# Kernel optimization log

Hardware: AMD Instinct MI355X
Metric: run time of the kernel (lower is better)

Reference implementation:

```python
import jax, jax.numpy as jnp
import numpy as np

HIDDEN = 1024

def _init_linear(key, in_f, out_f):
    kw, kb = jax.random.split(key)
    bound = 1.0 / np.sqrt(in_f)
    W = jax.random.uniform(kw, (out_f, in_f), jnp.float32, -bound, bound)
    b = jax.random.uniform(kb, (out_f,), jnp.float32, -bound, bound)
    return W, b

def setup_inputs() -> dict:
    key = jax.random.key(0)
    ks = jax.random.split(key, 6)
    x = jax.random.normal(ks[0], (64, 512, 512), jnp.float32)
    # layer 0: input_size=512, hidden=1024
    W_rz0, b_rz0 = _init_linear(ks[1], 512 + HIDDEN, 2 * HIDDEN)
    W_n0, b_n0 = _init_linear(ks[2], 512 + HIDDEN, HIDDEN)
    # layer 1: input_size=hidden=1024
    W_rz1, b_rz1 = _init_linear(ks[3], HIDDEN + HIDDEN, 2 * HIDDEN)
    W_n1, b_n1 = _init_linear(ks[4], HIDDEN + HIDDEN, HIDDEN)
    # final fc: hidden -> output_size=512
    W_fc, b_fc = _init_linear(ks[5], HIDDEN, 512)
    return {"x": x, "W_rz0": W_rz0, "b_rz0": b_rz0, "W_n0": W_n0, "b_n0": b_n0,
            "W_rz1": W_rz1, "b_rz1": b_rz1, "W_n1": W_n1, "b_n1": b_n1,
            "W_fc": W_fc, "b_fc": b_fc}

def _gru_cell(xt, h, W_rz, b_rz, W_n, b_n):
    ih = jnp.concatenate([xt, h], axis=1)                 # [B, in+H]
    rz = ih @ W_rz.T + b_rz                               # [B, 2H]
    r, z = jnp.split(rz, 2, axis=1)
    r = jax.nn.sigmoid(r)
    z = jax.nn.sigmoid(z)
    ih_n = jnp.concatenate([xt, r * h], axis=1)
    n = jnp.tanh(ih_n @ W_n.T + b_n)
    return (1.0 - z) * n + z * h

def reference(x, W_rz0, b_rz0, W_n0, b_n0, W_rz1, b_rz1, W_n1, b_n1, W_fc, b_fc):
    B = x.shape[0]
    h0 = jnp.zeros((B, HIDDEN), x.dtype)
    h1 = jnp.zeros((B, HIDDEN), x.dtype)

    def step(carry, xt):
        h0, h1 = carry
        h0 = _gru_cell(xt, h0, W_rz0, b_rz0, W_n0, b_n0)
        h1 = _gru_cell(h0, h1, W_rz1, b_rz1, W_n1, b_n1)
        return (h0, h1), None

    xs = jnp.swapaxes(x, 0, 1)                            # [T, B, in]
    (h0, h1), _ = jax.lax.scan(step, (h0, h1), xs)
    # original returns outputs[:, -1, :] == fc(final hidden of last layer)
    return h1 @ W_fc.T + b_fc
```

## Files before the change

### kernel.cpp

```cpp
#include <hip/hip_runtime.h>
#include <math.h>

typedef _Float16 h8 __attribute__((ext_vector_type(8)));
typedef float f4 __attribute__((ext_vector_type(4)));

#define H 1024

#define OFF_WRZ0 0ull
#define OFF_WN0  6291456ull
#define OFF_WRZ1 9437184ull
#define OFF_WN1  17825792ull
#define OFF_H0BF 22020096ull
#define OFF_H1BF 22282240ull
#define OFF_RH0  22544384ull
#define OFF_RH1  22675456ull
#define OFF_H0F  22806528ull
#define OFF_H1F  23068672ull
#define OFF_Z0F  23330816ull
#define OFF_Z1F  23592960ull
#define OFF_CNT  23855104ull
#define OFF_INFO 23856128ull
#define OFF_CCNT 23857152ull
#define OFF_CP   23863296ull
#define CP_XCD_STRIDE 655360ull
#define ZERO_WORDS 460800

__device__ __forceinline__ unsigned long long llc_ld64(const void* p) {
  return __hip_atomic_load((const unsigned long long*)p, __ATOMIC_RELAXED, __HIP_MEMORY_SCOPE_AGENT);
}
__device__ __forceinline__ void llc_st64(void* p, unsigned long long v) {
  __hip_atomic_store((unsigned long long*)p, v, __ATOMIC_RELAXED, __HIP_MEMORY_SCOPE_AGENT);
}
__device__ __forceinline__ void llc_st32(void* p, unsigned v) {
  __hip_atomic_store((unsigned*)p, v, __ATOMIC_RELAXED, __HIP_MEMORY_SCOPE_AGENT);
}
__device__ __forceinline__ unsigned long long pack2f(float a, float b) {
  union { float f[2]; unsigned long long u; } x; x.f[0] = a; x.f[1] = b; return x.u;
}
__device__ __forceinline__ void unpack2f(unsigned long long v, float& a, float& b) {
  union { unsigned long long u; float f[2]; } x; x.u = v; a = x.f[0]; b = x.f[1];
}
__device__ __forceinline__ unsigned packh2(float a, float b) {
  union { _Float16 h[2]; unsigned u; } x; x.h[0] = (_Float16)a; x.h[1] = (_Float16)b; return x.u;
}

__global__ __launch_bounds__(256) void prep_kernel(
    const float* __restrict__ wrz0f, const float* __restrict__ wn0f,
    const float* __restrict__ wrz1f, const float* __restrict__ wn1f,
    _Float16* __restrict__ wrz0, _Float16* __restrict__ wn0,
    _Float16* __restrict__ wrz1, _Float16* __restrict__ wn1,
    unsigned* __restrict__ zbase) {
  size_t i = (size_t)blockIdx.x * blockDim.x + threadIdx.x;
  size_t stride = (size_t)gridDim.x * blockDim.x;
  for (size_t k = i; k < 2048ull * 1536ull; k += stride) wrz0[k] = (_Float16)wrz0f[k];
  for (size_t k = i; k < 1024ull * 1536ull; k += stride) wn0[k]  = (_Float16)wn0f[k];
  for (size_t k = i; k < 2048ull * 2048ull; k += stride) wrz1[k] = (_Float16)wrz1f[k];
  for (size_t k = i; k < 1024ull * 2048ull; k += stride) wn1[k]  = (_Float16)wn1f[k];
  for (size_t k = i; k < (size_t)ZERO_WORDS; k += stride) zbase[k] = 0u;
}

__device__ __forceinline__ void wait_ge(unsigned long long* c, unsigned long long tgt) {
  if (threadIdx.x == 0) {
    int g = 0;
    while (__hip_atomic_load(c, __ATOMIC_RELAXED, __HIP_MEMORY_SCOPE_AGENT) < tgt) {
      if (++g > (1 << 21)) break;
      __builtin_amdgcn_s_sleep(2);
    }
  }
  __syncthreads();
}
__device__ __forceinline__ void signal(unsigned long long* c) {
  __syncthreads();
  if (threadIdx.x == 0)
    __hip_atomic_fetch_add(c, 1ull, __ATOMIC_RELAXED, __HIP_MEMORY_SCOPE_AGENT);
}

__device__ __forceinline__ void copy_tensor(const void* __restrict__ master,
                                            void* __restrict__ cp,
                                            int rank, int m,
                                            unsigned long long* ccnt,
                                            unsigned long long target) {
  const unsigned long long* src = (const unsigned long long*)master;
  unsigned long long* dst = (unsigned long long*)cp;
  for (int u = rank * 1024 + (int)threadIdx.x; u < 16384; u += m * 1024)
    dst[u] = llc_ld64(src + u);
  __syncthreads();
  if (threadIdx.x == 0) {
    __hip_atomic_fetch_add(ccnt, 1ull, __ATOMIC_RELAXED, __HIP_MEMORY_SCOPE_AGENT);
    int g = 0;
    while (__hip_atomic_load(ccnt, __ATOMIC_RELAXED, __HIP_MEMORY_SCOPE_AGENT) < target) {
      if (++g > (1 << 21)) break;
      __builtin_amdgcn_s_sleep(2);
    }
  }
  __syncthreads();
  asm volatile("buffer_inv sc0" ::: "memory");
}

template<int NT>
__device__ __forceinline__ void gemm_cp(const _Float16* __restrict__ A,
                                        const _Float16* const* wps, int coff, f4* acc) {
  const int lane = threadIdx.x & 63, wv = threadIdx.x >> 6;
  const int kwq = wv & 3, mw = wv >> 2;
  const int rsub = lane & 15, kg = (lane >> 4) << 3;
  const _Float16* ap = A + (size_t)(mw * 16 + rsub) * 1024 + kwq * 256 + kg;
#pragma unroll
  for (int k0 = 0; k0 < 256; k0 += 32) {
    h8 a = *(const h8*)(ap + k0);
    int kc = coff + kwq * 256 + k0 + kg;
#pragma unroll
    for (int c = 0; c < NT; ++c) {
      h8 wf = *(const h8*)(wps[c] + kc);
      acc[c] = __builtin_amdgcn_mfma_f32_16x16x32_f16(a, wf, acc[c], 0, 0, 0);
    }
  }
}

__device__ __forceinline__ void gemm_x(const float* __restrict__ x, int t,
                                       const _Float16* __restrict__ wr0,
                                       const _Float16* __restrict__ wr1,
                                       const _Float16* __restrict__ wn,
                                       f4* aRZ, f4* aN) {
  const int lane = threadIdx.x & 63, wv = threadIdx.x >> 6;
  const int kwq = wv & 3, mw = wv >> 2;
  const int rsub = lane & 15, kg = (lane >> 4) << 3;
  const float* xb = x + (size_t)(mw * 16 + rsub) * 262144 + (size_t)t * 512;
#pragma unroll
  for (int k0 = 0; k0 < 128; k0 += 32) {
    int k = kwq * 128 + k0 + kg;
    float4 f0 = *(const float4*)(xb + k);
    float4 f1 = *(const float4*)(xb + k + 4);
    h8 a;
    a[0] = (_Float16)f0.x; a[1] = (_Float16)f0.y; a[2] = (_Float16)f0.z; a[3] = (_Float16)f0.w;
    a[4] = (_Float16)f1.x; a[5] = (_Float16)f1.y; a[6] = (_Float16)f1.z; a[7] = (_Float16)f1.w;
    aRZ[0] = __builtin_amdgcn_mfma_f32_16x16x32_f16(a, *(const h8*)(wr0 + k), aRZ[0], 0, 0, 0);
    aRZ[1] = __builtin_amdgcn_mfma_f32_16x16x32_f16(a, *(const h8*)(wr1 + k), aRZ[1], 0, 0, 0);
    aN[0]  = __builtin_amdgcn_mfma_f32_16x16x32_f16(a, *(const h8*)(wn + k),  aN[0], 0, 0, 0);
  }
}

template<int NT>
__device__ __forceinline__ void red_write(float* __restrict__ red, const f4* acc) {
  const int lane = threadIdx.x & 63, wv = threadIdx.x >> 6;
  const int kwq = wv & 3, mw = wv >> 2;
  const int rsub = lane & 15, rg = lane >> 4;
#pragma unroll
  for (int c = 0; c < NT; ++c)
#pragma unroll
    for (int j = 0; j < 4; ++j)
      red[(size_t)(kwq * 64 + mw * 16 + rg * 4 + j) * 33 + c * 16 + rsub] = acc[c][j];
}

__device__ __forceinline__ void reduce_rz(const float* __restrict__ red, int cb,
    const float* __restrict__ bias, const float* __restrict__ hf,
    _Float16* __restrict__ rh, float* __restrict__ zf) {
  const int tid = threadIdx.x;
  const int row = tid >> 4, cp = (tid & 15) << 1;
  float v0 = 0.f, v1 = 0.f;
#pragma unroll
  for (int q = 0; q < 4; ++q) {
    const float* rr = red + (size_t)(q * 64 + row) * 33 + cp;
    v0 += rr[0]; v1 += rr[1];
  }
  v0 += bias[cb + cp]; v1 += bias[cb + cp + 1];
  float s0 = 1.f / (1.f + expf(-v0));
  float s1 = 1.f / (1.f + expf(-v1));
  if (cb < 1024) {
    float h0v, h1v;
    unpack2f(llc_ld64(hf + (size_t)row * H + cb + cp), h0v, h1v);
    llc_st32(rh + (size_t)row * H + cb + cp, packh2(s0 * h0v, s1 * h1v));
  } else {
    llc_st64(zf + (size_t)row * H + (cb - 1024) + cp, pack2f(s0, s1));
  }
}

__device__ __forceinline__ void reduce_n(const float* __restrict__ red, int nb,
    const float* __restrict__ bias, const float* __restrict__ zf,
    float* __restrict__ hf, _Float16* __restrict__ hb) {
  const int tid = threadIdx.x;
  if (tid < 512) {
    const int row = tid >> 3, cp = (tid & 7) << 1;
    float v0 = 0.f, v1 = 0.f;
#pragma unroll
    for (int q = 0; q < 4; ++q) {
      const float* rr = red + (size_t)(q * 64 + row) * 33 + cp;
      v0 += rr[0]; v1 += rr[1];
    }
    v0 += bias[nb + cp]; v1 += bias[nb + cp + 1];
    float n0 = tanhf(v0), n1 = tanhf(v1);
    float z0, z1, h0v, h1v;
    unpack2f(llc_ld64(zf + (size_t)row * H + nb + cp), z0, z1);
    unpack2f(llc_ld64(hf + (size_t)row * H + nb + cp), h0v, h1v);
    float o0 = (1.f - z0) * n0 + z0 * h0v;
    float o1 = (1.f - z1) * n1 + z1 * h1v;
    llc_st64(hf + (size_t)row * H + nb + cp, pack2f(o0, o1));
    llc_st32(hb + (size_t)row * H + nb + cp, packh2(o0, o1));
  }
}

__global__ __launch_bounds__(1024) void gru_main(const float* __restrict__ x,
    const _Float16* __restrict__ wrz0, const _Float16* __restrict__ wn0,
    const _Float16* __restrict__ wrz1, const _Float16* __restrict__ wn1,
    const float* __restrict__ brz0, const float* __restrict__ bn0,
    const float* __restrict__ brz1, const float* __restrict__ bn1,
    _Float16* __restrict__ h0bf, _Float16* __restrict__ h1bf,
    _Float16* __restrict__ rh0, _Float16* __restrict__ rh1,
    float* __restrict__ h0f, float* __restrict__ h1f,
    float* __restrict__ z0f, float* __restrict__ z1f,
    unsigned long long* __restrict__ cnt, unsigned* __restrict__ info,
    unsigned long long* __restrict__ ccnt_all, char* __restrict__ cpbase) {
  __shared__ float red[256 * 33];
  __shared__ int sh_meta[3];
  const int bid = blockIdx.x;
  const int tid = threadIdx.x;
  const int myrole = (bid < 64) ? 0 : 1;

  if (tid == 0) {
    unsigned xcc;
    asm volatile("s_getreg_b32 %0, hwreg(HW_REG_XCC_ID)" : "=s"(xcc));
    xcc &= 7u;
    llc_st32(&info[bid], 0x100u | xcc);
    asm volatile("s_waitcnt vmcnt(0)" ::: "memory");
    __hip_atomic_fetch_add(&cnt[4], 1ull, __ATOMIC_RELAXED, __HIP_MEMORY_SCOPE_AGENT);
    int g = 0;
    while (__hip_atomic_load(&cnt[4], __ATOMIC_RELAXED, __HIP_MEMORY_SCOPE_AGENT) < 128ull) {
      if (++g > (1 << 22)) break;
      __builtin_amdgcn_s_sleep(2);
    }
    int rankR = 0, mR = 0;
    for (int b = 0; b < 128; ++b) {
      unsigned v = (unsigned)__hip_atomic_load(&info[b], __ATOMIC_RELAXED, __HIP_MEMORY_SCOPE_AGENT);
      if ((v & 7u) == xcc && ((b < 64) ? 0 : 1) == myrole) {
        if (b < bid) rankR++;
        mR++;
      }
    }
    sh_meta[0] = (int)xcc; sh_meta[1] = rankR; sh_meta[2] = mR;
  }
  __syncthreads();
  const int xcd = sh_meta[0], rankR = sh_meta[1], mR = sh_meta[2];
  unsigned long long* cc = ccnt_all + (size_t)xcd * 5 * 16;
  char* cpx = cpbase + (size_t)xcd * CP_XCD_STRIDE;
  _Float16* cpS[5];
#pragma unroll
  for (int i = 0; i < 5; ++i) cpS[i] = (_Float16*)(cpx + (size_t)i * 131072);
  const int rsub = tid & 15;

  if (myrole == 0) {
    const int cb = bid * 32, nb = bid * 16;
    const _Float16* wpsRZ[2] = { wrz0 + (size_t)(cb + rsub) * 1536,
                                 wrz0 + (size_t)(cb + 16 + rsub) * 1536 };
    const _Float16* wpsN[1] = { wn0 + (size_t)(nb + rsub) * 1536 };
    for (int t = 0; t < 512; ++t) {
      f4 aRZ[2] = { f4{0.f,0.f,0.f,0.f}, f4{0.f,0.f,0.f,0.f} };
      f4 aN[1] = { f4{0.f,0.f,0.f,0.f} };
      gemm_x(x, t, wpsRZ[0], wpsRZ[1], wpsN[0], aRZ, aN);
      wait_ge(&cnt[1], 64ull * (unsigned long long)t);
      if (t >= 1) {
        copy_tensor(h0bf + (size_t)((t - 1) & 1) * 65536, cpS[0],
                    rankR, mR, &cc[0 * 16], (unsigned long long)mR * t);
        gemm_cp<2>(cpS[0], wpsRZ, 512, aRZ);
      }
      red_write<2>(red, aRZ);
      __syncthreads();
      reduce_rz(red, cb, brz0, h0f, rh0, z0f);
      signal(&cnt[0]);
      wait_ge(&cnt[0], 64ull * (unsigned long long)(t + 1));
      if (t >= 1) wait_ge(&cnt[3], 64ull * (unsigned long long)(t - 1));
      if (t >= 1) {
        copy_tensor(rh0, cpS[1], rankR, mR, &cc[1 * 16], (unsigned long long)mR * t);
        gemm_cp<1>(cpS[1], wpsN, 512, aN);
      }
      red_write<1>(red, aN);
      __syncthreads();
      reduce_n(red, nb, bn0, z0f, h0f, h0bf + (size_t)(t & 1) * 65536);
      signal(&cnt[1]);
    }
  } else {
    const int b = bid - 64, cb = b * 32, nb = b * 16;
    const _Float16* wps3[3] = { wrz1 + (size_t)(cb + rsub) * 2048,
                                wrz1 + (size_t)(cb + 16 + rsub) * 2048,
                                wn1  + (size_t)(nb + rsub) * 2048 };
    for (int t = 1; t <= 512; ++t) {
      const int s = t - 1;
      f4 acc3[3] = { f4{0.f,0.f,0.f,0.f}, f4{0.f,0.f,0.f,0.f}, f4{0.f,0.f,0.f,0.f} };
      wait_ge(&cnt[3], 64ull * (unsigned long long)s);
      if (s >= 1) {
        copy_tensor(h1bf + (size_t)((s - 1) & 1) * 65536, cpS[2],
                    rankR, mR, &cc[2 * 16], (unsigned long long)mR * s);
        gemm_cp<2>(cpS[2], wps3, 1024, acc3);
      }
      wait_ge(&cnt[1], 64ull * (unsigned long long)t);
      copy_tensor(h0bf + (size_t)((t - 1) & 1) * 65536, cpS[3],
                  rankR, mR, &cc[3 * 16], (unsigned long long)mR * t);
      gemm_cp<3>(cpS[3], wps3, 0, acc3);
      red_write<2>(red, acc3);
      __syncthreads();
      reduce_rz(red, cb, brz1, h1f, rh1, z1f);
      signal(&cnt[2]);
      wait_ge(&cnt[2], 64ull * (unsigned long long)t);
      if (s >= 1) {
        copy_tensor(rh1, cpS[4], rankR, mR, &cc[4 * 16], (unsigned long long)mR * s);
        gemm_cp<1>(cpS[4], wps3 + 2, 1024, acc3 + 2);
      }
      red_write<1>(red, acc3 + 2);
      __syncthreads();
      reduce_n(red, nb, bn1, z1f, h1f, h1bf + (size_t)(s & 1) * 65536);
      signal(&cnt[3]);
    }
  }
}

__global__ __launch_bounds__(256) void fc_kernel(const float* __restrict__ h1f,
                                                 const float* __restrict__ wfc,
                                                 const float* __restrict__ bfc,
                                                 float* __restrict__ out) {
  const int bid = blockIdx.x;
#pragma unroll
  for (int rep = 0; rep < 2; ++rep) {
    int local = threadIdx.x + rep * 256;
    int b = local >> 3;
    int o = bid * 8 + (local & 7);
    const float4* hp = (const float4*)(h1f + (size_t)b * 1024);
    const float4* wp = (const float4*)(wfc + (size_t)o * 1024);
    float s = 0.f;
#pragma unroll 4
    for (int i2 = 0; i2 < 256; ++i2) {
      float4 hv = hp[i2], wv = wp[i2];
      s += hv.x * wv.x + hv.y * wv.y + hv.z * wv.z + hv.w * wv.w;
    }
    out[(size_t)b * 512 + o] = s + bfc[o];
  }
}

extern "C" void kernel_launch(void* const* d_in, const int* in_sizes, int n_in,
                              void* d_out, int out_size, void* d_ws, size_t ws_size,
                              hipStream_t stream) {
  const float* x    = (const float*)d_in[0];
  const float* Wrz0 = (const float*)d_in[1];
  const float* brz0 = (const float*)d_in[2];
  const float* Wn0  = (const float*)d_in[3];
  const float* bn0  = (const float*)d_in[4];
  const float* Wrz1 = (const float*)d_in[5];
  const float* brz1 = (const float*)d_in[6];
  const float* Wn1  = (const float*)d_in[7];
  const float* bn1  = (const float*)d_in[8];
  const float* Wfc  = (const float*)d_in[9];
  const float* bfc  = (const float*)d_in[10];
  float* out = (float*)d_out;
  char* ws = (char*)d_ws;

  _Float16* wrz0h = (_Float16*)(ws + OFF_WRZ0);
  _Float16* wn0h  = (_Float16*)(ws + OFF_WN0);
  _Float16* wrz1h = (_Float16*)(ws + OFF_WRZ1);
  _Float16* wn1h  = (_Float16*)(ws + OFF_WN1);
  _Float16* h0bf  = (_Float16*)(ws + OFF_H0BF);
  _Float16* h1bf  = (_Float16*)(ws + OFF_H1BF);
  _Float16* rh0   = (_Float16*)(ws + OFF_RH0);
  _Float16* rh1   = (_Float16*)(ws + OFF_RH1);
  float* h0f = (float*)(ws + OFF_H0F);
  float* h1f = (float*)(ws + OFF_H1F);
  float* z0f = (float*)(ws + OFF_Z0F);
  float* z1f = (float*)(ws + OFF_Z1F);
  unsigned long long* cnt = (unsigned long long*)(ws + OFF_CNT);
  unsigned* info = (unsigned*)(ws + OFF_INFO);
  unsigned long long* ccnt = (unsigned long long*)(ws + OFF_CCNT);
  char* cpbase = ws + OFF_CP;

  prep_kernel<<<2048, 256, 0, stream>>>(Wrz0, Wn0, Wrz1, Wn1,
                                        wrz0h, wn0h, wrz1h, wn1h,
                                        (unsigned*)(ws + OFF_H0BF));
  gru_main<<<128, 1024, 0, stream>>>(x, wrz0h, wn0h, wrz1h, wn1h,
                                     brz0, bn0, brz1, bn1,
                                     h0bf, h1bf, rh0, rh1,
                                     h0f, h1f, z0f, z1f,
                                     cnt, info, ccnt, cpbase);
  fc_kernel<<<64, 256, 0, stream>>>(h1f, Wfc, bfc, out);
}
```

Before: 23.03 ms.

## Split copy into issue and crew-sync, merge layer-1 copies, prefetch gate operands

Splits the per-XCD replica copy into a separate issue phase and a crew barrier. In layer 1 the two input copies (h1 and h0) now share a single crew barrier instead of each having its own, removing one cross-block sync per step. It also loads the h and z values needed by the gate epilogues right after the wait, before the GEMM, so their global-load latency is hidden behind compute. The risk is more ordering subtlety: the h1 copy now depends on the later crew_sync for visibility, and the values held in registers for longer raise register pressure.

```diff
diff --git a/kernel.cpp b/kernel.cpp
--- a/kernel.cpp
+++ b/kernel.cpp
@@ -3,6 +3,7 @@
 
 typedef _Float16 h8 __attribute__((ext_vector_type(8)));
 typedef float f4 __attribute__((ext_vector_type(4)));
+typedef unsigned long long u64;
 
 #define H 1024
 
@@ -25,20 +26,20 @@
 #define CP_XCD_STRIDE 655360ull
 #define ZERO_WORDS 460800
 
-__device__ __forceinline__ unsigned long long llc_ld64(const void* p) {
-  return __hip_atomic_load((const unsigned long long*)p, __ATOMIC_RELAXED, __HIP_MEMORY_SCOPE_AGENT);
-}
-__device__ __forceinline__ void llc_st64(void* p, unsigned long long v) {
-  __hip_atomic_store((unsigned long long*)p, v, __ATOMIC_RELAXED, __HIP_MEMORY_SCOPE_AGENT);
+__device__ __forceinline__ u64 llc_ld64(const void* p) {
+  return __hip_atomic_load((const u64*)p, __ATOMIC_RELAXED, __HIP_MEMORY_SCOPE_AGENT);
+}
+__device__ __forceinline__ void llc_st64(void* p, u64 v) {
+  __hip_atomic_store((u64*)p, v, __ATOMIC_RELAXED, __HIP_MEMORY_SCOPE_AGENT);
 }
 __device__ __forceinline__ void llc_st32(void* p, unsigned v) {
   __hip_atomic_store((unsigned*)p, v, __ATOMIC_RELAXED, __HIP_MEMORY_SCOPE_AGENT);
 }
-__device__ __forceinline__ unsigned long long pack2f(float a, float b) {
-  union { float f[2]; unsigned long long u; } x; x.f[0] = a; x.f[1] = b; return x.u;
-}
-__device__ __forceinline__ void unpack2f(unsigned long long v, float& a, float& b) {
-  union { unsigned long long u; float f[2]; } x; x.u = v; a = x.f[0]; b = x.f[1];
+__device__ __forceinline__ u64 pack2f(float a, float b) {
+  union { float f[2]; u64 u; } x; x.f[0] = a; x.f[1] = b; return x.u;
+}
+__device__ __forceinline__ void unpack2f(u64 v, float& a, float& b) {
+  union { u64 u; float f[2]; } x; x.u = v; a = x.f[0]; b = x.f[1];
 }
 __device__ __forceinline__ unsigned packh2(float a, float b) {
   union { _Float16 h[2]; unsigned u; } x; x.h[0] = (_Float16)a; x.h[1] = (_Float16)b; return x.u;
@@ -59,7 +60,7 @@
   for (size_t k = i; k < (size_t)ZERO_WORDS; k += stride) zbase[k] = 0u;
 }
 
-__device__ __forceinline__ void wait_ge(unsigned long long* c, unsigned long long tgt) {
+__device__ __forceinline__ void wait_ge(u64* c, u64 tgt) {
   if (threadIdx.x == 0) {
     int g = 0;
     while (__hip_atomic_load(c, __ATOMIC_RELAXED, __HIP_MEMORY_SCOPE_AGENT) < tgt) {
@@ -69,21 +70,20 @@
   }
   __syncthreads();
 }
-__device__ __forceinline__ void signal(unsigned long long* c) {
+__device__ __forceinline__ void signal(u64* c) {
   __syncthreads();
   if (threadIdx.x == 0)
     __hip_atomic_fetch_add(c, 1ull, __ATOMIC_RELAXED, __HIP_MEMORY_SCOPE_AGENT);
 }
 
-__device__ __forceinline__ void copy_tensor(const void* __restrict__ master,
-                                            void* __restrict__ cp,
-                                            int rank, int m,
-                                            unsigned long long* ccnt,
-                                            unsigned long long target) {
-  const unsigned long long* src = (const unsigned long long*)master;
-  unsigned long long* dst = (unsigned long long*)cp;
+__device__ __forceinline__ void copy_issue(const void* __restrict__ master,
+                                           void* __restrict__ cp, int rank, int m) {
+  const u64* src = (const u64*)master;
+  u64* dst = (u64*)cp;
   for (int u = rank * 1024 + (int)threadIdx.x; u < 16384; u += m * 1024)
     dst[u] = llc_ld64(src + u);
+}
+__device__ __forceinline__ void crew_sync(u64* ccnt, u64 target) {
   __syncthreads();
   if (threadIdx.x == 0) {
     __hip_atomic_fetch_add(ccnt, 1ull, __ATOMIC_RELAXED, __HIP_MEMORY_SCOPE_AGENT);
@@ -151,8 +151,23 @@
       red[(size_t)(kwq * 64 + mw * 16 + rg * 4 + j) * 33 + c * 16 + rsub] = acc[c][j];
 }
 
+__device__ __forceinline__ u64 pre_rz(const float* __restrict__ hf, int cb) {
+  if (cb >= 1024) return 0ull;
+  int row = threadIdx.x >> 4, cp = (threadIdx.x & 15) << 1;
+  return llc_ld64(hf + (size_t)row * H + cb + cp);
+}
+__device__ __forceinline__ void pre_n(const float* __restrict__ zf,
+                                      const float* __restrict__ hf, int nb,
+                                      u64& zv, u64& hv) {
+  if (threadIdx.x < 512) {
+    int row = threadIdx.x >> 3, cp = (threadIdx.x & 7) << 1;
+    zv = llc_ld64(zf + (size_t)row * H + nb + cp);
+    hv = llc_ld64(hf + (size_t)row * H + nb + cp);
+  }
+}
+
 __device__ __forceinline__ void reduce_rz(const float* __restrict__ red, int cb,
-    const float* __restrict__ bias, const float* __restrict__ hf,
+    const float* __restrict__ bias, u64 hpre,
     _Float16* __restrict__ rh, float* __restrict__ zf) {
   const int tid = threadIdx.x;
   const int row = tid >> 4, cp = (tid & 15) << 1;
@@ -167,7 +182,7 @@
   float s1 = 1.f / (1.f + expf(-v1));
   if (cb < 1024) {
     float h0v, h1v;
-    unpack2f(llc_ld64(hf + (size_t)row * H + cb + cp), h0v, h1v);
+    unpack2f(hpre, h0v, h1v);
     llc_st32(rh + (size_t)row * H + cb + cp, packh2(s0 * h0v, s1 * h1v));
   } else {
     llc_st64(zf + (size_t)row * H + (cb - 1024) + cp, pack2f(s0, s1));
@@ -175,7 +190,7 @@
 }
 
 __device__ __forceinline__ void reduce_n(const float* __restrict__ red, int nb,
-    const float* __restrict__ bias, const float* __restrict__ zf,
+    const float* __restrict__ bias, u64 zpre, u64 hpre,
     float* __restrict__ hf, _Float16* __restrict__ hb) {
   const int tid = threadIdx.x;
   if (tid < 512) {
@@ -189,8 +204,8 @@
     v0 += bias[nb + cp]; v1 += bias[nb + cp + 1];
     float n0 = tanhf(v0), n1 = tanhf(v1);
     float z0, z1, h0v, h1v;
-    unpack2f(llc_ld64(zf + (size_t)row * H + nb + cp), z0, z1);
-    unpack2f(llc_ld64(hf + (size_t)row * H + nb + cp), h0v, h1v);
+    unpack2f(zpre, z0, z1);
+    unpack2f(hpre, h0v, h1v);
     float o0 = (1.f - z0) * n0 + z0 * h0v;
     float o1 = (1.f - z1) * n1 + z1 * h1v;
     llc_st64(hf + (size_t)row * H + nb + cp, pack2f(o0, o1));
@@ -207,8 +222,8 @@
     _Float16* __restrict__ rh0, _Float16* __restrict__ rh1,
     float* __restrict__ h0f, float* __restrict__ h1f,
     float* __restrict__ z0f, float* __restrict__ z1f,
-    unsigned long long* __restrict__ cnt, unsigned* __restrict__ info,
-    unsigned long long* __restrict__ ccnt_all, char* __restrict__ cpbase) {
+    u64* __restrict__ cnt, unsigned* __restrict__ info,
+    u64* __restrict__ ccnt_all, char* __restrict__ cpbase) {
   __shared__ float red[256 * 33];
   __shared__ int sh_meta[3];
   const int bid = blockIdx.x;
@@ -239,7 +254,7 @@
   }
   __syncthreads();
   const int xcd = sh_meta[0], rankR = sh_meta[1], mR = sh_meta[2];
-  unsigned long long* cc = ccnt_all + (size_t)xcd * 5 * 16;
+  u64* cc = ccnt_all + (size_t)xcd * 5 * 16;
   char* cpx = cpbase + (size_t)xcd * CP_XCD_STRIDE;
   _Float16* cpS[5];
 #pragma unroll
@@ -255,25 +270,29 @@
       f4 aRZ[2] = { f4{0.f,0.f,0.f,0.f}, f4{0.f,0.f,0.f,0.f} };
       f4 aN[1] = { f4{0.f,0.f,0.f,0.f} };
       gemm_x(x, t, wpsRZ[0], wpsRZ[1], wpsN[0], aRZ, aN);
-      wait_ge(&cnt[1], 64ull * (unsigned long long)t);
+      wait_ge(&cnt[1], 64ull * (u64)t);
+      u64 hpre = pre_rz(h0f, cb);
       if (t >= 1) {
-        copy_tensor(h0bf + (size_t)((t - 1) & 1) * 65536, cpS[0],
-                    rankR, mR, &cc[0 * 16], (unsigned long long)mR * t);
+        copy_issue(h0bf + (size_t)((t - 1) & 1) * 65536, cpS[0], rankR, mR);
+        crew_sync(&cc[0 * 16], (u64)mR * t);
         gemm_cp<2>(cpS[0], wpsRZ, 512, aRZ);
       }
       red_write<2>(red, aRZ);
       __syncthreads();
-      reduce_rz(red, cb, brz0, h0f, rh0, z0f);
+      reduce_rz(red, cb, brz0, hpre, rh0, z0f);
       signal(&cnt[0]);
-      wait_ge(&cnt[0], 64ull * (unsigned long long)(t + 1));
-      if (t >= 1) wait_ge(&cnt[3], 64ull * (unsigned long long)(t - 1));
+      wait_ge(&cnt[0], 64ull * (u64)(t + 1));
+      if (t >= 1) wait_ge(&cnt[3], 64ull * (u64)(t - 1));
+      u64 zpre = 0, hpre2 = 0;
+      pre_n(z0f, h0f, nb, zpre, hpre2);
       if (t >= 1) {
-        copy_tensor(rh0, cpS[1], rankR, mR, &cc[1 * 16], (unsigned long long)mR * t);
+        copy_issue(rh0, cpS[1], rankR, mR);
+        crew_sync(&cc[1 * 16], (u64)mR * t);
         gemm_cp<1>(cpS[1], wpsN, 512, aN);
       }
       red_write<1>(red, aN);
       __syncthreads();
-      reduce_n(red, nb, bn0, z0f, h0f, h0bf + (size_t)(t & 1) * 65536);
+      reduce_n(red, nb, bn0, zpre, hpre2, h0f, h0bf + (size_t)(t & 1) * 65536);
       signal(&cnt[1]);
     }
   } else {
@@ -284,28 +303,30 @@
     for (int t = 1; t <= 512; ++t) {
       const int s = t - 1;
       f4 acc3[3] = { f4{0.f,0.f,0.f,0.f}, f4{0.f,0.f,0.f,0.f}, f4{0.f,0.f,0.f,0.f} };
-      wait_ge(&cnt[3], 64ull * (unsigned long long)s);
-      if (s >= 1) {
-        copy_tensor(h1bf + (size_t)((s - 1) & 1) * 65536, cpS[2],
-                    rankR, mR, &cc[2 * 16], (unsigned long long)mR * s);
-        gemm_cp<2>(cpS[2], wps3, 1024, acc3);
-      }
-      wait_ge(&cnt[1], 64ull * (unsigned long long)t);
-      copy_tensor(h0bf + (size_t)((t - 1) & 1) * 65536, cpS[3],
-                  rankR, mR, &cc[3 * 16], (unsigned long long)mR * t);
+      wait_ge(&cnt[3], 64ull * (u64)s);
+      u64 hpre = pre_rz(h1f, cb);
+      if (s >= 1)
+        copy_issue(h1bf + (size_t)((s - 1) & 1) * 65536, cpS[2], rankR, mR);
+      wait_ge(&cnt[1], 64ull * (u64)t);
+      copy_issue(h0bf + (size_t)((t - 1) & 1) * 65536, cpS[3], rankR, mR);
+      crew_sync(&cc[3 * 16], (u64)mR * t);
+      if (s >= 1) gemm_cp<2>(cpS[2], wps3, 1024, acc3);
       gemm_cp<3>(cpS[3], wps3, 0, acc3);
       red_write<2>(red, acc3);
       __syncthreads();
-      reduce_rz(red, cb, brz1, h1f, rh1, z1f);
+      reduce_rz(red, cb, brz1, hpre, rh1, z1f);
       signal(&cnt[2]);
-      wait_ge(&cnt[2], 64ull * (unsigned long long)t);
+      wait_ge(&cnt[2], 64ull * (u64)t);
+      u64 zpre = 0, hpre2 = 0;
+      pre_n(z1f, h1f, nb, zpre, hpre2);
       if (s >= 1) {
-        copy_tensor(rh1, cpS[4], rankR, mR, &cc[4 * 16], (unsigned long long)mR * s);
+        copy_issue(rh1, cpS[4], rankR, mR);
+        crew_sync(&cc[4 * 16], (u64)mR * s);
         gemm_cp<1>(cpS[4], wps3 + 2, 1024, acc3 + 2);
       }
       red_write<1>(red, acc3 + 2);
       __syncthreads();
-      reduce_n(red, nb, bn1, z1f, h1f, h1bf + (size_t)(s & 1) * 65536);
+      reduce_n(red, nb, bn1, zpre, hpre2, h1f, h1bf + (size_t)(s & 1) * 65536);
       signal(&cnt[3]);
     }
   }
@@ -362,9 +383,9 @@
   float* h1f = (float*)(ws + OFF_H1F);
   float* z0f = (float*)(ws + OFF_Z0F);
   float* z1f = (float*)(ws + OFF_Z1F);
-  unsigned long long* cnt = (unsigned long long*)(ws + OFF_CNT);
+  u64* cnt = (u64*)(ws + OFF_CNT);
   unsigned* info = (unsigned*)(ws + OFF_INFO);
-  unsigned long long* ccnt = (unsigned long long*)(ws + OFF_CCNT);
+  u64* ccnt = (u64*)(ws + OFF_CCNT);
   char* cpbase = ws + OFF_CP;
 
   prep_kernel<<<2048, 256, 0, stream>>>(Wrz0, Wn0, Wrz1, Wn1,
```

After: 22.25 ms. 1.03x faster.
